# Optimization experiments

Hardware: AMD Instinct MI355X
Metric: run time of the kernel (lower is better)

Reference implementation:

```python
import jax, jax.numpy as jnp
import numpy as np
from itertools import product

C_IN, C_OUT = 32, 64
N_DOWN = 100000
CHILD = 4
N = N_DOWN * CHILD  # 400000 active voxels


def _encode(c):
    # pack nonnegative (x,y,z) voxel coords into a single int64 key
    c = c.astype(np.int64)
    return (c[:, 0] << 40) | (c[:, 1] << 20) | c[:, 2]


def _build_coords(rng):
    # N_DOWN unique parent voxels in [1,126]^3, each with exactly CHILD distinct children
    flat = rng.choice(126 ** 3, N_DOWN, replace=False)
    px = flat // (126 * 126) + 1
    py = (flat // 126) % 126 + 1
    pz = flat % 126 + 1
    parents = np.stack([px, py, pz], 1)  # [N_DOWN,3]
    child_off = rng.random((N_DOWN, 8)).argsort(1)[:, :CHILD]  # [N_DOWN,4] in 0..7
    bits = np.stack([child_off >> 2 & 1, child_off >> 1 & 1, child_off & 1], -1)  # [N_DOWN,4,3]
    children = (2 * parents[:, None, :] + bits).reshape(N, 3)
    kvec = child_off.reshape(N)  # kernel offset id of each child within its parent
    parent_of = np.repeat(np.arange(N_DOWN), CHILD)
    return children, kvec, parent_of


def _build_kmap3(children):
    # submanifold 3x3x3 neighbor map: km_in[k,i] = index j with coords[j] = coords[i] + off_k
    keys = _encode(children)
    order = np.argsort(keys)
    skeys = keys[order]
    offsets = list(product((-1, 0, 1), repeat=3))
    km_in = np.full((27, N), N, np.int32)
    km_out = np.full((27, N), N, np.int32)
    ar = np.arange(N, dtype=np.int32)
    for k, off in enumerate(offsets):
        nk = _encode(children + np.asarray(off))
        pos = np.clip(np.searchsorted(skeys, nk), 0, N - 1)
        found = skeys[pos] == nk
        km_in[k] = np.where(found, order[pos].astype(np.int32), N)
        km_out[k] = np.where(found, ar, N)
    return km_in, km_out


def _build_kmap_pool(kvec, parent_of):
    # kernel-2 stride-2 conv: each child feeds exactly one parent at offset kvec
    kp_in = np.full((8, N), N, np.int32)
    kp_out = np.full((8, N), N_DOWN, np.int32)
    for k in range(8):
        idx = np.nonzero(kvec == k)[0]
        kp_in[k, :len(idx)] = idx
        kp_out[k, :len(idx)] = parent_of[idx]
    return kp_in, kp_out


def setup_inputs() -> dict:
    rng = np.random.default_rng(0)
    children, kvec, parent_of = _build_coords(rng)
    km_in, km_out = _build_kmap3(children)
    kp_in, kp_out = _build_kmap_pool(kvec, parent_of)

    key = jax.random.key(0)
    ks = jax.random.split(key, 10)
    f32 = jnp.float32
    return {
        'x': jax.random.normal(ks[0], (N, C_IN), f32),
        'W1': jax.random.normal(ks[1], (27, C_IN, C_OUT), f32) * 0.05,
        'bn1_s': jax.random.uniform(ks[2], (C_OUT,), f32, 0.5, 1.5),
        'bn1_b': jax.random.normal(ks[3], (C_OUT,), f32) * 0.1,
        'W2': jax.random.normal(ks[4], (27, C_OUT, C_OUT), f32) * 0.05,
        'bn2_s': jax.random.uniform(ks[5], (C_OUT,), f32, 0.5, 1.5),
        'bn2_b': jax.random.normal(ks[6], (C_OUT,), f32) * 0.1,
        'Wp': jax.random.normal(ks[7], (8, C_OUT, C_OUT), f32) * 0.05,
        'bnp_s': jax.random.uniform(ks[8], (C_OUT,), f32, 0.5, 1.5),
        'bnp_b': jax.random.normal(ks[9], (C_OUT,), f32) * 0.1,
        'km_in': jnp.asarray(km_in),
        'km_out': jnp.asarray(km_out),
        'kp_in': jnp.asarray(kp_in),
        'kp_out': jnp.asarray(kp_out),
        'n_down': N_DOWN,
    }


def _sparse_conv(x, W, iidx, oidx, n_out):
    # gather -> per-offset matmul -> scatter-add; invalid pairs point at zero row / dump row
    xp = jnp.concatenate([x, jnp.zeros((1, x.shape[1]), x.dtype)], 0)
    def body(acc, a):
        Wk, ii, oi = a
        return acc.at[oi].add(xp[ii] @ Wk), None
    acc0 = jnp.zeros((n_out + 1, W.shape[2]), x.dtype)
    acc, _ = jax.lax.scan(body, acc0, (W, iidx, oidx))
    return acc[:n_out]


def _bn_relu(h, s, b):
    return jax.nn.relu(h * s + b)


def reference(x, W1, bn1_s, bn1_b, W2, bn2_s, bn2_b, Wp, bnp_s, bnp_b,
              km_in, km_out, kp_in, kp_out, n_down):
    n = x.shape[0]
    h = _bn_relu(_sparse_conv(x, W1, km_in, km_out, n), bn1_s, bn1_b)
    down = _bn_relu(_sparse_conv(h, W2, km_in, km_out, n), bn2_s, bn2_b)
    p = _bn_relu(_sparse_conv(down, Wp, kp_in, kp_out, n_down), bnp_s, bnp_b)
    return (down, p)
```

## Files before the change

### kernel.cpp

```cpp
#include <hip/hip_runtime.h>


#define NV 400000
#define ND 100000

typedef __attribute__((ext_vector_type(8))) short  bf16x8;
typedef __attribute__((ext_vector_type(4))) float  f32x4;

__device__ __forceinline__ unsigned short f2b(float f) {
    unsigned int u = __builtin_bit_cast(unsigned int, f);
    u += 0x7fffu + ((u >> 16) & 1u);
    return (unsigned short)(u >> 16);
}

__global__ __launch_bounds__(256) void cvt_bf16_k(
    const float* __restrict__ in, unsigned short* __restrict__ out, int n)
{
    int t = (blockIdx.x * 256 + threadIdx.x) * 4;
    if (t >= n) return;
    float4 f = *(const float4*)(in + t);
    ushort4 u;
    u.x = f2b(f.x); u.y = f2b(f.y); u.z = f2b(f.z); u.w = f2b(f.w);
    *(ushort4*)(out + t) = u;
}

__global__ __launch_bounds__(256) void pack_w_k(
    const float* __restrict__ W, unsigned short* __restrict__ out, int nk, int ci)
{
    int t = blockIdx.x * 256 + threadIdx.x;
    int steps = ci >> 5;
    if (t >= nk * steps * 4 * 64) return;
    int lane = t & 63;
    int nt   = (t >> 6) & 3;
    int rest = t >> 8;
    int s    = rest % steps;
    int k    = rest / steps;
    int col = lane & 15, quad = lane >> 4;
    int co = nt * 16 + col;
    unsigned short v[8];
#pragma unroll
    for (int j = 0; j < 8; ++j) {
        int cidx = s * 32 + quad * 8 + j;
        v[j] = f2b(W[((size_t)k * ci + cidx) * 64 + co]);
    }
    bf16x8 frag;
#pragma unroll
    for (int j = 0; j < 8; ++j) frag[j] = (short)v[j];
    *(bf16x8*)(out + (size_t)t * 8) = frag;
}

__global__ __launch_bounds__(256) void ck_init_k(int* __restrict__ ck)
{
    int t = blockIdx.x * 256 + threadIdx.x;
    if (t < ND * 8) ck[t] = NV;
}
__global__ __launch_bounds__(256) void ck_scatter_k(
    const int* __restrict__ kp_in, const int* __restrict__ kp_out,
    int* __restrict__ ck)
{
    int t = blockIdx.x * 256 + threadIdx.x;
    if (t >= 8 * NV) return;
    int j = kp_in[t];
    if (j == NV) return;
    int k = t / NV;
    ck[(size_t)k * ND + kp_out[t]] = j;
}

template <int CI, int NK, int MODE, int NR>
__device__ __forceinline__ void conv_body(
    const unsigned short* __restrict__ xin,
    const unsigned short* __restrict__ Wp,
    const int* __restrict__ km,
    const float* __restrict__ bns, const float* __restrict__ bnb,
    float* __restrict__ outf, unsigned short* __restrict__ outb)
{
    constexpr int STEPS = CI / 32;
    constexpr int FR = STEPS * 4;
    __shared__ unsigned short bsh[2 * FR * 512];
    __shared__ int jsh[2][256];

    const int lane = threadIdx.x & 63;
    const int wave = threadIdx.x >> 6;
    const int col = lane & 15, quad = lane >> 4;

    const int nwg = gridDim.x;
    const int q = nwg >> 3, r = nwg & 7;
    const int xcd = blockIdx.x & 7, bodd = blockIdx.x >> 3;
    const int bid = (xcd < r ? xcd * (q + 1) : r * (q + 1) + (xcd - r) * q) + bodd;

    const int wbase = (bid * 4 + wave) * 64;

    const int srow = (wbase + lane < NR) ? wbase + lane : NR - 1;

    f32x4 acc[4][4];
#pragma unroll
    for (int mt = 0; mt < 4; ++mt)
#pragma unroll
        for (int nt = 0; nt < 4; ++nt) acc[mt][nt] = (f32x4)0.f;

    auto stage = [&](int k, int b) {
#pragma unroll
        for (int f = wave; f < FR; f += 4) {
            const unsigned short* src = Wp + ((size_t)(k * FR + f) * 64 + lane) * 8;
            __builtin_amdgcn_global_load_lds(
                (const __attribute__((address_space(1))) void*)src,
                (__attribute__((address_space(3))) void*)&bsh[b * (FR * 512) + f * 512],
                16, 0, 0);
        }
        const int* psrc = km + (size_t)k * NR + srow;
        __builtin_amdgcn_global_load_lds(
            (const __attribute__((address_space(1))) void*)psrc,
            (__attribute__((address_space(3))) void*)&jsh[b][wave * 64],
            4, 0, 0);
    };

    stage(0, 0);
    int buf = 0;

    for (int k = 0; k < NK; ++k) {
        __syncthreads();
        if (k + 1 < NK) stage(k + 1, buf ^ 1);

        int j[4];
#pragma unroll
        for (int mt = 0; mt < 4; ++mt)
            j[mt] = jsh[buf][wave * 64 + mt * 16 + col];

#pragma unroll
        for (int s = 0; s < STEPS; ++s) {
            bf16x8 a[4];
#pragma unroll
            for (int mt = 0; mt < 4; ++mt)
                a[mt] = *(const bf16x8*)(xin + (size_t)j[mt] * CI + s * 32 + quad * 8);
#pragma unroll
            for (int nt = 0; nt < 4; ++nt) {
                bf16x8 b = *(const bf16x8*)&bsh[buf * (FR * 512) + (s * 4 + nt) * 512 + lane * 8];
#pragma unroll
                for (int mt = 0; mt < 4; ++mt)
                    acc[mt][nt] = __builtin_amdgcn_mfma_f32_16x16x32_bf16(
                        a[mt], b, acc[mt][nt], 0, 0, 0);
            }
        }
        buf ^= 1;
    }

#pragma unroll
    for (int nt = 0; nt < 4; ++nt) {
        const int n = nt * 16 + col;
        const float sc = bns[n], bi = bnb[n];
#pragma unroll
        for (int mt = 0; mt < 4; ++mt)
#pragma unroll
            for (int rr = 0; rr < 4; ++rr) {
                int row = wbase + mt * 16 + quad * 4 + rr;
                if (row < NR) {
                    float v = fmaxf(fmaf(acc[mt][nt][rr], sc, bi), 0.f);
                    if constexpr (MODE == 0) {
                        outf[(size_t)row * 64 + n] = v;
                    } else if constexpr (MODE == 1) {
                        outb[(size_t)row * 64 + n] = f2b(v);
                    } else {
                        outf[(size_t)row * 64 + n] = v;
                        outb[(size_t)row * 64 + n] = f2b(v);
                    }
                }
            }
    }
}

__global__ __launch_bounds__(256) void conv1_k(
    const unsigned short* __restrict__ xin, const unsigned short* __restrict__ Wp,
    const int* __restrict__ km, const float* __restrict__ bns,
    const float* __restrict__ bnb, unsigned short* __restrict__ outb)
{
    conv_body<32, 27, 1, NV>(xin, Wp, km, bns, bnb, nullptr, outb);
}
__global__ __launch_bounds__(256) void conv2_k(
    const unsigned short* __restrict__ xin, const unsigned short* __restrict__ Wp,
    const int* __restrict__ km, const float* __restrict__ bns,
    const float* __restrict__ bnb, float* __restrict__ outf,
    unsigned short* __restrict__ outb)
{
    conv_body<64, 27, 2, NV>(xin, Wp, km, bns, bnb, outf, outb);
}
__global__ __launch_bounds__(256) void pool_k(
    const unsigned short* __restrict__ xin, const unsigned short* __restrict__ Wp,
    const int* __restrict__ ck, const float* __restrict__ bns,
    const float* __restrict__ bnb, float* __restrict__ outf)
{
    conv_body<64, 8, 0, ND>(xin, Wp, ck, bns, bnb, outf, nullptr);
}

extern "C" void kernel_launch(void* const* d_in, const int* in_sizes, int n_in,
                              void* d_out, int out_size, void* d_ws, size_t ws_size,
                              hipStream_t stream)
{
    const float* x    = (const float*)d_in[0];
    const float* W1   = (const float*)d_in[1];
    const float* bn1s = (const float*)d_in[2];
    const float* bn1b = (const float*)d_in[3];
    const float* W2   = (const float*)d_in[4];
    const float* bn2s = (const float*)d_in[5];
    const float* bn2b = (const float*)d_in[6];
    const float* Wp   = (const float*)d_in[7];
    const float* bnps = (const float*)d_in[8];
    const float* bnpb = (const float*)d_in[9];
    const int* km_in  = (const int*)d_in[10];
    const int* kp_in  = (const int*)d_in[12];
    const int* kp_out = (const int*)d_in[13];

    float* down = (float*)d_out;
    float* pout = (float*)d_out + (size_t)NV * 64;

    char* ws = (char*)d_ws;
    unsigned short* x_bf  = (unsigned short*)ws;  ws += (size_t)(NV + 1) * 32 * 2;
    unsigned short* h_bf  = (unsigned short*)ws;  ws += (size_t)(NV + 1) * 64 * 2;
    unsigned short* d_bf  = (unsigned short*)ws;  ws += (size_t)(NV + 1) * 64 * 2;
    int*            ck    = (int*)ws;             ws += (size_t)8 * ND * 4;
    unsigned short* W1p   = (unsigned short*)ws;  ws += (size_t)27 * 32 * 64 * 2;
    unsigned short* W2p   = (unsigned short*)ws;  ws += (size_t)27 * 64 * 64 * 2;
    unsigned short* Wpp   = (unsigned short*)ws;

    hipMemsetAsync(x_bf + (size_t)NV * 32, 0, 32 * 2, stream);
    hipMemsetAsync(h_bf + (size_t)NV * 64, 0, 64 * 2, stream);
    hipMemsetAsync(d_bf + (size_t)NV * 64, 0, 64 * 2, stream);

    cvt_bf16_k<<<(NV * 32 / 4 + 255) / 256, 256, 0, stream>>>(x, x_bf, NV * 32);
    pack_w_k<<<(27 * 1 * 4 * 64 + 255) / 256, 256, 0, stream>>>(W1, W1p, 27, 32);
    pack_w_k<<<(27 * 2 * 4 * 64 + 255) / 256, 256, 0, stream>>>(W2, W2p, 27, 64);
    pack_w_k<<<(8  * 2 * 4 * 64 + 255) / 256, 256, 0, stream>>>(Wp, Wpp, 8, 64);
    ck_init_k<<<(ND * 8 + 255) / 256, 256, 0, stream>>>(ck);
    ck_scatter_k<<<(8 * NV + 255) / 256, 256, 0, stream>>>(kp_in, kp_out, ck);

    const int cgrid = (NV + 255) / 256;
    conv1_k<<<cgrid, 256, 0, stream>>>(x_bf, W1p, km_in, bn1s, bn1b, h_bf);
    conv2_k<<<cgrid, 256, 0, stream>>>(h_bf, W2p, km_in, bn2s, bn2b, down, d_bf);
    pool_k<<<(ND + 255) / 256, 256, 0, stream>>>(d_bf, Wpp, ck, bnps, bnpb, pout);
}
```

Baseline: 609.9 us.

## Prefetch next offset's gathered activations into registers and merge weight packing kernels

```diff
diff --git a/kernel.cpp b/kernel.cpp
--- a/kernel.cpp
+++ b/kernel.cpp
@@ -24,12 +24,11 @@
     *(ushort4*)(out + t) = u;
 }
 
-__global__ __launch_bounds__(256) void pack_w_k(
-    const float* __restrict__ W, unsigned short* __restrict__ out, int nk, int ci)
-{
-    int t = blockIdx.x * 256 + threadIdx.x;
+__device__ __forceinline__ void pack_one(
+    const float* __restrict__ W, unsigned short* __restrict__ out,
+    int ci, int t)
+{
     int steps = ci >> 5;
-    if (t >= nk * steps * 4 * 64) return;
     int lane = t & 63;
     int nt   = (t >> 6) & 3;
     int rest = t >> 8;
@@ -37,16 +36,26 @@
     int k    = rest / steps;
     int col = lane & 15, quad = lane >> 4;
     int co = nt * 16 + col;
-    unsigned short v[8];
+    bf16x8 frag;
 #pragma unroll
     for (int j = 0; j < 8; ++j) {
         int cidx = s * 32 + quad * 8 + j;
-        v[j] = f2b(W[((size_t)k * ci + cidx) * 64 + co]);
-    }
-    bf16x8 frag;
-#pragma unroll
-    for (int j = 0; j < 8; ++j) frag[j] = (short)v[j];
+        frag[j] = (short)f2b(W[((size_t)k * ci + cidx) * 64 + co]);
+    }
     *(bf16x8*)(out + (size_t)t * 8) = frag;
+}
+__global__ __launch_bounds__(256) void pack_all_k(
+    const float* __restrict__ W1, unsigned short* __restrict__ W1p,
+    const float* __restrict__ W2, unsigned short* __restrict__ W2p,
+    const float* __restrict__ Wp, unsigned short* __restrict__ Wpp)
+{
+    int t = blockIdx.x * 256 + threadIdx.x;
+    constexpr int N1 = 27 * 1 * 4 * 64;
+    constexpr int N2 = 27 * 2 * 4 * 64;
+    constexpr int N3 = 8  * 2 * 4 * 64;
+    if (t < N1)                 pack_one(W1, W1p, 32, t);
+    else if (t < N1 + N2)       pack_one(W2, W2p, 64, t - N1);
+    else if (t < N1 + N2 + N3)  pack_one(Wp, Wpp, 64, t - N1 - N2);
 }
 
 __global__ __launch_bounds__(256) void ck_init_k(int* __restrict__ ck)
@@ -98,7 +107,7 @@
 #pragma unroll
         for (int nt = 0; nt < 4; ++nt) acc[mt][nt] = (f32x4)0.f;
 
-    auto stage = [&](int k, int b) {
+    auto stage_b = [&](int k, int b) {
 #pragma unroll
         for (int f = wave; f < FR; f += 4) {
             const unsigned short* src = Wp + ((size_t)(k * FR + f) * 64 + lane) * 8;
@@ -107,42 +116,68 @@
                 (__attribute__((address_space(3))) void*)&bsh[b * (FR * 512) + f * 512],
                 16, 0, 0);
         }
+    };
+    auto stage_km = [&](int k) {
         const int* psrc = km + (size_t)k * NR + srow;
         __builtin_amdgcn_global_load_lds(
             (const __attribute__((address_space(1))) void*)psrc,
-            (__attribute__((address_space(3))) void*)&jsh[b][wave * 64],
+            (__attribute__((address_space(3))) void*)&jsh[k & 1][wave * 64],
             4, 0, 0);
     };
 
-    stage(0, 0);
-    int buf = 0;
-
-    for (int k = 0; k < NK; ++k) {
-        __syncthreads();
-        if (k + 1 < NK) stage(k + 1, buf ^ 1);
-
-        int j[4];
+    stage_b(0, 0);
+    stage_km(0);
+    stage_km(1);
+    __syncthreads();
+
+    bf16x8 aP[STEPS][4], aQ[STEPS][4];
+    {
+        int j0[4];
 #pragma unroll
         for (int mt = 0; mt < 4; ++mt)
-            j[mt] = jsh[buf][wave * 64 + mt * 16 + col];
-
-#pragma unroll
-        for (int s = 0; s < STEPS; ++s) {
-            bf16x8 a[4];
+            j0[mt] = jsh[0][wave * 64 + mt * 16 + col];
+#pragma unroll
+        for (int s = 0; s < STEPS; ++s)
 #pragma unroll
             for (int mt = 0; mt < 4; ++mt)
-                a[mt] = *(const bf16x8*)(xin + (size_t)j[mt] * CI + s * 32 + quad * 8);
+                aP[s][mt] = *(const bf16x8*)(
+                    xin + (size_t)j0[mt] * CI + s * 32 + quad * 8);
+    }
+
+    auto body = [&](int k, bf16x8 (&aIn)[STEPS][4], bf16x8 (&aOut)[STEPS][4]) {
+        if (k + 1 < NK) {
+            int jn[4];
+#pragma unroll
+            for (int mt = 0; mt < 4; ++mt)
+                jn[mt] = jsh[(k + 1) & 1][wave * 64 + mt * 16 + col];
+#pragma unroll
+            for (int s = 0; s < STEPS; ++s)
+#pragma unroll
+                for (int mt = 0; mt < 4; ++mt)
+                    aOut[s][mt] = *(const bf16x8*)(
+                        xin + (size_t)jn[mt] * CI + s * 32 + quad * 8);
+            stage_b(k + 1, (k + 1) & 1);
+            if (k + 2 < NK) stage_km(k + 2);
+        }
+#pragma unroll
+        for (int s = 0; s < STEPS; ++s)
 #pragma unroll
             for (int nt = 0; nt < 4; ++nt) {
-                bf16x8 b = *(const bf16x8*)&bsh[buf * (FR * 512) + (s * 4 + nt) * 512 + lane * 8];
+                bf16x8 b = *(const bf16x8*)&bsh[(k & 1) * (FR * 512)
+                                                + (s * 4 + nt) * 512 + lane * 8];
 #pragma unroll
                 for (int mt = 0; mt < 4; ++mt)
                     acc[mt][nt] = __builtin_amdgcn_mfma_f32_16x16x32_bf16(
-                        a[mt], b, acc[mt][nt], 0, 0, 0);
+                        aIn[s][mt], b, acc[mt][nt], 0, 0, 0);
             }
-        }
-        buf ^= 1;
-    }
+        __syncthreads();
+    };
+
+    for (int kk = 0; kk < NK / 2; ++kk) {
+        body(2 * kk,     aP, aQ);
+        body(2 * kk + 1, aQ, aP);
+    }
+    if constexpr (NK & 1) body(NK - 1, aP, aQ);
 
 #pragma unroll
     for (int nt = 0; nt < 4; ++nt) {
@@ -168,14 +203,14 @@
     }
 }
 
-__global__ __launch_bounds__(256) void conv1_k(
+__global__ __launch_bounds__(256, 2) void conv1_k(
     const unsigned short* __restrict__ xin, const unsigned short* __restrict__ Wp,
     const int* __restrict__ km, const float* __restrict__ bns,
     const float* __restrict__ bnb, unsigned short* __restrict__ outb)
 {
     conv_body<32, 27, 1, NV>(xin, Wp, km, bns, bnb, nullptr, outb);
 }
-__global__ __launch_bounds__(256) void conv2_k(
+__global__ __launch_bounds__(256, 2) void conv2_k(
     const unsigned short* __restrict__ xin, const unsigned short* __restrict__ Wp,
     const int* __restrict__ km, const float* __restrict__ bns,
     const float* __restrict__ bnb, float* __restrict__ outf,
@@ -183,7 +218,7 @@
 {
     conv_body<64, 27, 2, NV>(xin, Wp, km, bns, bnb, outf, outb);
 }
-__global__ __launch_bounds__(256) void pool_k(
+__global__ __launch_bounds__(256, 2) void pool_k(
     const unsigned short* __restrict__ xin, const unsigned short* __restrict__ Wp,
     const int* __restrict__ ck, const float* __restrict__ bns,
     const float* __restrict__ bnb, float* __restrict__ outf)
@@ -226,9 +261,8 @@
     hipMemsetAsync(d_bf + (size_t)NV * 64, 0, 64 * 2, stream);
 
     cvt_bf16_k<<<(NV * 32 / 4 + 255) / 256, 256, 0, stream>>>(x, x_bf, NV * 32);
-    pack_w_k<<<(27 * 1 * 4 * 64 + 255) / 256, 256, 0, stream>>>(W1, W1p, 27, 32);
-    pack_w_k<<<(27 * 2 * 4 * 64 + 255) / 256, 256, 0, stream>>>(W2, W2p, 27, 64);
-    pack_w_k<<<(8  * 2 * 4 * 64 + 255) / 256, 256, 0, stream>>>(Wp, Wpp, 8, 64);
+    pack_all_k<<<(27 * 4 * 64 * 3 + 8 * 2 * 4 * 64 + 255) / 256, 256, 0, stream>>>(
+        W1, W1p, W2, W2p, Wp, Wpp);
     ck_init_k<<<(ND * 8 + 255) / 256, 256, 0, stream>>>(ck);
     ck_scatter_k<<<(8 * NV + 255) / 256, 256, 0, stream>>>(kp_in, kp_out, ck);
 
```

Result: faster. 589.7 us (-3.3%).
